# Optimization experiments

Measured on AMD Instinct MI355X. Metric: run time of the kernel, lower is better.

The kernel has to match this reference:

```python
import jax, jax.numpy as jnp
import numpy as np

jax.config.update("jax_enable_x64", True)

ZDNA_COORDS = np.array([
    [19.907, 16.823, 19.09], [18.239, 15.35, 17.81], [19.352, 12.428, 20.252],
    [19.86, 12.683, 22.751], [17.43, 10.434, 25.869], [15.111, 11.013, 24.853],
    [13.376, 8.973, 27.734], [14.066, 8.488, 30.129], [11.402, 9.495, 33.572],
    [10.614, 11.665, 32.479], [8.13, 12.128, 35.334], [8.074, 11.534, 37.812]],
    dtype=np.float32)

SIGMA_ALIGN = 5.0
WEIGHT = 10.0
MAX_ITER = 10
BINDERLEN = 400000


def _center_coords(coords):
    centered = coords - coords.mean(axis=0, keepdims=True)
    # torch .std() is unbiased (ddof=1)
    std = jnp.clip(centered.std(axis=0, ddof=1).mean(), 1e-6, None)
    return centered / std


def _soft_assignment(P, Q, sigma):
    # squared euclidean distances: [12, N]
    d2 = (jnp.sum(Q * Q, axis=1)[:, None] + jnp.sum(P * P, axis=1)[None, :]
          - 2.0 * Q @ P.T)
    d2 = jnp.maximum(d2, 0.0)
    W = jnp.exp(-d2 / (2.0 * sigma ** 2 + 1e-6))
    return W / (W.sum(axis=1, keepdims=True) + 1e-6)


def _weighted_kabsch(P, Q, W):
    dtype = P.dtype
    Pd, Qd, Wd = P.astype(jnp.float64), Q.astype(jnp.float64), W.astype(jnp.float64)
    w_sum = jnp.clip(Wd.sum(), 1e-6, None)
    centroid_P = Wd.sum(axis=0) @ Pd / w_sum   # [3]
    centroid_Q = Wd.sum(axis=1) @ Qd / w_sum   # [3]
    P_cent = Pd - centroid_P                   # [N,3]
    Q_cent = Qd - centroid_Q                   # [12,3]
    H = P_cent.T @ (Wd.T @ Q_cent)             # [3,3]
    H = H + jnp.eye(3, dtype=jnp.float64) * 1e-6
    U, _, Vh = jnp.linalg.svd(H, full_matrices=False)
    R = Vh.T @ U.T
    R = R * jnp.sign(jnp.linalg.det(R))
    t = centroid_Q - centroid_P @ R
    return R.astype(dtype), t.astype(dtype)


def _robust_alignment(P, Q, sigma, max_iter=MAX_ITER):
    Q_current = Q
    prev_rmsd = jnp.array(jnp.inf, dtype=P.dtype)  # never updated in original
    rmsd = prev_rmsd
    for _ in range(max_iter):
        W = _soft_assignment(P, Q_current)         # [12,N]
        R, t = _weighted_kabsch(P, Q_current, W)
        Q_new = Q_current @ R + t                  # [12,3]
        residuals = jnp.linalg.norm(Q_new - W @ P, axis=1)
        rmsd = jnp.sqrt(jnp.mean(residuals ** 2) + 1e-6)
        Q_current = Q_new
        rmsd = jnp.where(prev_rmsd < rmsd, prev_rmsd, rmsd)
    return rmsd


def _soft_assignment(P, Q, sigma=SIGMA_ALIGN):
    d2 = (jnp.sum(Q * Q, axis=1)[:, None] + jnp.sum(P * P, axis=1)[None, :]
          - 2.0 * Q @ P.T)
    d2 = jnp.maximum(d2, 0.0)
    W = jnp.exp(-d2 / (2.0 * sigma ** 2 + 1e-6))
    return W / (W.sum(axis=1, keepdims=True) + 1e-6)


def setup_inputs() -> dict:
    key = jax.random.key(0)
    k1, = jax.random.split(key, 1)
    xyz = jax.random.normal(k1, (BINDERLEN, 27, 3), dtype=jnp.float32) * 10.0
    zdna_ref = jnp.asarray(ZDNA_COORDS)
    return {"xyz": xyz, "zdna_ref": zdna_ref, "binderlen": BINDERLEN}


def reference(xyz, zdna_ref, binderlen):
    binder_ca = xyz[:binderlen, 1]           # [N,3]
    binder_norm = _center_coords(binder_ca)
    zdna_norm = _center_coords(zdna_ref)     # [12,3]
    rmsd = _robust_alignment(binder_norm, zdna_norm, SIGMA_ALIGN)
    return -WEIGHT * rmsd
```

## Files before the change

### kernel.cpp

```cpp
#include <hip/hip_runtime.h>
#include <math.h>

#define NBLK 256
#define THREADS 256
#define PTS 7
#define NSHARD 8
#define CPAD 16
#define KORD 5
#define MORD 6
#define NMOM 84
#define NCON 56
#define CC 50.000001

__device__ double g_slot[NBLK][8];
__device__ double g_macc[NSHARD][NMOM];
__device__ int g_cnt[2 * CPAD];

__device__ inline float waveReduceAdd(float v) {
#pragma unroll
    for (int off = 32; off > 0; off >>= 1) v += __shfl_down(v, off, 64);
    return v;
}

__device__ inline int loadRlxI(int* p) {
    return __hip_atomic_load(p, __ATOMIC_RELAXED, __HIP_MEMORY_SCOPE_AGENT);
}
__device__ inline int loadAcqI(int* p) {
    return __hip_atomic_load(p, __ATOMIC_ACQUIRE, __HIP_MEMORY_SCOPE_AGENT);
}
__device__ inline double loadRlxD(double* p) {
    return __hip_atomic_load(p, __ATOMIC_RELAXED, __HIP_MEMORY_SCOPE_AGENT);
}
__device__ inline void storeRlxD(double* p, double v) {
    __hip_atomic_store(p, v, __ATOMIC_RELAXED, __HIP_MEMORY_SCOPE_AGENT);
}

__device__ inline void arriveAndWait(int slot, int target) {
    __threadfence();
    atomicAdd(&g_cnt[slot * CPAD], 1);
    while (loadRlxI(&g_cnt[slot * CPAD]) < target) __builtin_amdgcn_s_sleep(8);
    (void)loadAcqI(&g_cnt[slot * CPAD]);
}

__device__ inline int idx6(int a, int b, int g) {
    int off = 0;
    for (int ap = 0; ap < a; ++ap) off += (7 - ap) * (8 - ap) / 2;
    return off + b * (7 - a) - b * (b - 1) / 2 + g;
}

__device__ void kabschUpdate(const double* __restrict__ dsum,
                             double (*Qd)[3], float (*Qf)[3],
                             float* __restrict__ out, int it) {
    double S[12], Tv[12][3], Q[12][3];
    for (int i = 0; i < 12; i++) {
        S[i] = dsum[i];
        Tv[i][0] = dsum[12 + i];
        Tv[i][1] = dsum[24 + i];
        Tv[i][2] = dsum[36 + i];
        for (int c = 0; c < 3; c++) Q[i][c] = Qd[i][c];
    }
    double n[12], wsum = 0;
    for (int i = 0; i < 12; i++) {
        n[i] = 1.0 / (S[i] + 1e-6);
        wsum += S[i] * n[i];
    }
    wsum = fmax(wsum, 1e-6);
    double cP[3] = {0, 0, 0}, cQ[3] = {0, 0, 0};
    for (int i = 0; i < 12; i++)
        for (int c = 0; c < 3; c++) {
            cP[c] += n[i] * Tv[i][c];
            cQ[c] += S[i] * n[i] * Q[i][c];
        }
    for (int c = 0; c < 3; c++) { cP[c] /= wsum; cQ[c] /= wsum; }

    double H[3][3] = {{0, 0, 0}, {0, 0, 0}, {0, 0, 0}};
    for (int i = 0; i < 12; i++) {
        double ta[3];
        for (int a = 0; a < 3; a++) ta[a] = n[i] * (Tv[i][a] - S[i] * cP[a]);
        for (int a = 0; a < 3; a++)
            for (int b = 0; b < 3; b++) H[a][b] += ta[a] * (Q[i][b] - cQ[b]);
    }
    for (int a = 0; a < 3; a++) H[a][a] += 1e-6;

    double A[3][3], V[3][3];
    for (int a = 0; a < 3; a++)
        for (int b = 0; b < 3; b++) {
            double s = 0;
            for (int k = 0; k < 3; k++) s += H[k][a] * H[k][b];
            A[a][b] = s;
            V[a][b] = (a == b) ? 1.0 : 0.0;
        }
    for (int sweep = 0; sweep < 8; sweep++) {
        for (int p = 0; p < 2; p++)
            for (int q = p + 1; q < 3; q++) {
                double apq = A[p][q];
                if (fabs(apq) < 1e-12 * (fabs(A[p][p]) + fabs(A[q][q]))) continue;
                double theta = (A[q][q] - A[p][p]) / (2.0 * apq);
                double t = copysign(1.0, theta) / (fabs(theta) + sqrt(theta * theta + 1.0));
                double c = 1.0 / sqrt(t * t + 1.0);
                double s = t * c;
                A[p][p] = A[p][p] - t * apq;
                A[q][q] = A[q][q] + t * apq;
                A[p][q] = 0; A[q][p] = 0;
                int r = 3 - p - q;
                double arp = A[r][p], arq = A[r][q];
                A[r][p] = A[p][r] = c * arp - s * arq;
                A[r][q] = A[q][r] = s * arp + c * arq;
                for (int k = 0; k < 3; k++) {
                    double vkp = V[k][p], vkq = V[k][q];
                    V[k][p] = c * vkp - s * vkq;
                    V[k][q] = s * vkp + c * vkq;
                }
            }
    }
    double U[3][3];
    for (int k = 0; k < 3; k++) {
        double sig = sqrt(fmax(A[k][k], 0.0));
        double u[3];
        for (int a = 0; a < 3; a++)
            u[a] = H[a][0] * V[0][k] + H[a][1] * V[1][k] + H[a][2] * V[2][k];
        double invsig = 1.0 / fmax(sig, 1e-30);
        for (int a = 0; a < 3; a++) U[a][k] = u[a] * invsig;
    }
    double R[3][3];
    for (int a = 0; a < 3; a++)
        for (int b = 0; b < 3; b++)
            R[a][b] = V[a][0] * U[b][0] + V[a][1] * U[b][1] + V[a][2] * U[b][2];
    double det = R[0][0] * (R[1][1] * R[2][2] - R[1][2] * R[2][1])
               - R[0][1] * (R[1][0] * R[2][2] - R[1][2] * R[2][0])
               + R[0][2] * (R[1][0] * R[2][1] - R[1][1] * R[2][0]);
    if (det < 0)
        for (int a = 0; a < 3; a++)
            for (int b = 0; b < 3; b++) R[a][b] = -R[a][b];
    double tr[3];
    for (int b = 0; b < 3; b++)
        tr[b] = cQ[b] - (cP[0] * R[0][b] + cP[1] * R[1][b] + cP[2] * R[2][b]);

    double res2 = 0;
    for (int i = 0; i < 12; i++) {
        double qn[3];
        for (int b = 0; b < 3; b++) {
            qn[b] = Q[i][0] * R[0][b] + Q[i][1] * R[1][b] + Q[i][2] * R[2][b] + tr[b];
            double diff = qn[b] - n[i] * Tv[i][b];
            res2 += diff * diff;
        }
        for (int b = 0; b < 3; b++) {
            Qd[i][b] = qn[b];
            Qf[i][b] = (float)qn[b];
        }
    }
    if (it == 9) {
        double rmsd = sqrt(res2 / 12.0 + 1e-6);
        out[0] = (float)(-10.0 * rmsd);
    }
}

__global__ void __launch_bounds__(THREADS)
k_all(const float* __restrict__ xyz, const float* __restrict__ zdna,
      float* __restrict__ out, int N) {
    const int tid = threadIdx.x, bid = blockIdx.x;
    const int gid = bid * THREADS + tid;
    const int gsz = NBLK * THREADS;
    const int wave = tid >> 6, lane = tid & 63;

    __shared__ int s_base;
    __shared__ double shPart[4][NMOM];
    __shared__ double red8[8][6];
    __shared__ double Md[NMOM];
    __shared__ double coefL[NCON];
    __shared__ int lutL[4][NCON];
    __shared__ double lds48[48];
    __shared__ double QdL[12][3];
    __shared__ float QfL[12][3];
    __shared__ float s_mean[3], s_inv;

    if (tid == 0) s_base = loadRlxI(&g_cnt[CPAD]);
    __syncthreads();
    const int target = s_base + NBLK;

    float px[PTS], py[PTS], pz[PTS];
    float s0 = 0, s1 = 0, s2 = 0, q0 = 0, q1 = 0, q2 = 0;
#pragma unroll
    for (int k = 0; k < PTS; k++) {
        int j = gid + k * gsz;
        px[k] = 0.0f; py[k] = 0.0f; pz[k] = 0.0f;
        if (j < N) {
            size_t b = (size_t)j * 81 + 3;
            float x = xyz[b + 0], y = xyz[b + 1], z = xyz[b + 2];
            px[k] = x; py[k] = y; pz[k] = z;
            s0 += x; s1 += y; s2 += z;
            q0 += x * x; q1 += y * y; q2 += z * z;
        }
    }
    {
        float v[6] = {s0, s1, s2, q0, q1, q2};
#pragma unroll
        for (int k = 0; k < 6; k++) v[k] = waveReduceAdd(v[k]);
        if (lane == 0) {
#pragma unroll
            for (int k = 0; k < 6; k++) shPart[wave][k] = (double)v[k];
        }
        __syncthreads();
        if (tid < 6)
            storeRlxD(&g_slot[bid][tid],
                      shPart[0][tid] + shPart[1][tid] + shPart[2][tid] + shPart[3][tid]);
        if (bid < NSHARD && tid < NMOM) storeRlxD(&g_macc[bid][tid], 0.0);
        if (tid < NMOM) __threadfence();
        __syncthreads();
        if (tid == 0) arriveAndWait(0, target);
        __syncthreads();
    }

    {
        if (tid < 48) {
            int col = tid % 6, seg = tid / 6;
            double a0 = 0, a1 = 0;
            for (int b2 = seg * 32; b2 < seg * 32 + 32; b2 += 2) {
                a0 += loadRlxD(&g_slot[b2][col]);
                a1 += loadRlxD(&g_slot[b2 + 1][col]);
            }
            red8[seg][col] = a0 + a1;
        }
        __syncthreads();
        if (tid == 0) {
            double tot[6];
            for (int c = 0; c < 6; c++) {
                double s = 0;
                for (int g = 0; g < 8; g++) s += red8[g][c];
                tot[c] = s;
            }
            double mean[3], stdsum = 0;
            for (int c = 0; c < 3; c++) {
                mean[c] = tot[c] / (double)N;
                double var = (tot[3 + c] - (double)N * mean[c] * mean[c]) / (double)(N - 1);
                stdsum += sqrt(fmax(var, 0.0));
            }
            double sdev = fmax(stdsum / 3.0, 1e-6);
            s_mean[0] = (float)mean[0];
            s_mean[1] = (float)mean[1];
            s_mean[2] = (float)mean[2];
            s_inv = (float)(1.0 / sdev);

            double z[12][3], zm[3] = {0, 0, 0};
            for (int i = 0; i < 12; i++)
                for (int c = 0; c < 3; c++) {
                    z[i][c] = (double)zdna[i * 3 + c];
                    zm[c] += z[i][c];
                }
            for (int c = 0; c < 3; c++) zm[c] /= 12.0;
            double zvar[3] = {0, 0, 0};
            for (int i = 0; i < 12; i++)
                for (int c = 0; c < 3; c++) {
                    z[i][c] -= zm[c];
                    zvar[c] += z[i][c] * z[i][c];
                }
            double zs = 0;
            for (int c = 0; c < 3; c++) zs += sqrt(zvar[c] / 11.0);
            zs = fmax(zs / 3.0, 1e-6);
            double zinv = 1.0 / zs;
            for (int i = 0; i < 12; i++)
                for (int c = 0; c < 3; c++) {
                    double q = z[i][c] * zinv;
                    QdL[i][c] = q;
                    QfL[i][c] = (float)q;
                }
        }
        __syncthreads();
    }

    {
        float mx = s_mean[0], my = s_mean[1], mz = s_mean[2];
        float inv = s_inv;
#pragma unroll
        for (int k = 0; k < PTS; k++) {
            px[k] = (px[k] - mx) * inv;
            py[k] = (py[k] - my) * inv;
            pz[k] = (pz[k] - mz) * inv;
        }
    }

    {
        float mom[NMOM];
#pragma unroll
        for (int k = 0; k < NMOM; k++) mom[k] = 0.0f;
#pragma unroll
        for (int k = 0; k < PTS; k++) {
            if (gid + k * gsz < N) {
                float x = px[k], y = py[k], z = pz[k];
                float pp = x * x + y * y + z * z;
                float w0 = __expf(-pp * (float)(1.0 / CC));
                float ta = w0;
                int m = 0;
#pragma unroll
                for (int a = 0; a <= MORD; ++a) {
                    float tb = ta;
#pragma unroll
                    for (int b = 0; b <= MORD - a; ++b) {
                        float tc = tb;
#pragma unroll
                        for (int g = 0; g <= MORD - a - b; ++g) {
                            mom[m] += tc;
                            tc *= z;
                            ++m;
                        }
                        tb *= y;
                    }
                    ta *= x;
                }
            }
        }
#pragma unroll
        for (int k = 0; k < NMOM; k++) mom[k] = waveReduceAdd(mom[k]);
        if (lane == 0) {
#pragma unroll
            for (int k = 0; k < NMOM; k++) shPart[wave][k] = (double)mom[k];
        }
        __syncthreads();
        if (tid < NMOM) {
            double s = shPart[0][tid] + shPart[1][tid] + shPart[2][tid] + shPart[3][tid];
            (void)__hip_atomic_fetch_add(&g_macc[bid & (NSHARD - 1)][tid], s,
                                         __ATOMIC_RELAXED, __HIP_MEMORY_SCOPE_AGENT);
            __threadfence();
        }
        __syncthreads();
    }

    if (bid != 0) {
        if (tid == 0) {
            __threadfence();
            atomicAdd(&g_cnt[CPAD], 1);
        }
        return;
    }
    if (tid == 0) arriveAndWait(1, target);
    __syncthreads();

    if (tid < NMOM) {
        double s = 0;
#pragma unroll
        for (int s8 = 0; s8 < NSHARD; ++s8) s += loadRlxD(&g_macc[s8][tid]);
        Md[tid] = s;
    }
    if (tid == 64) {
        int m = 0;
        for (int a = 0; a <= KORD; ++a)
            for (int b = 0; b <= KORD - a; ++b)
                for (int g = 0; g <= KORD - a - b; ++g) {
                    double c = 1.0;
                    for (int t = 0; t < a + b + g; ++t) c *= 2.0 / CC;
                    for (int t = 2; t <= a; ++t) c /= (double)t;
                    for (int t = 2; t <= b; ++t) c /= (double)t;
                    for (int t = 2; t <= g; ++t) c /= (double)t;
                    coefL[m] = c;
                    lutL[0][m] = idx6(a, b, g);
                    lutL[1][m] = idx6(a + 1, b, g);
                    lutL[2][m] = idx6(a, b + 1, g);
                    lutL[3][m] = idx6(a, b, g + 1);
                    ++m;
                }
    }
    __syncthreads();

    for (int it = 0; it < 10; ++it) {
        if (tid < 48) {
            int i = tid >> 2, comp = tid & 3;
            double qx = (double)QfL[i][0];
            double qy = (double)QfL[i][1];
            double qz = (double)QfL[i][2];
            double acc = 0.0;
            int m = 0;
            double xa = 1.0;
            for (int a = 0; a <= KORD; ++a) {
                double yb = xa;
                for (int b = 0; b <= KORD - a; ++b) {
                    double zg = yb;
                    for (int g = 0; g <= KORD - a - b; ++g) {
                        acc += coefL[m] * zg * Md[lutL[comp][m]];
                        zg *= qz;
                        ++m;
                    }
                    yb *= qy;
                }
                xa *= qx;
            }
            double qq = qx * qx + qy * qy + qz * qz;
            lds48[comp * 12 + i] = exp(-qq / CC) * acc;
        }
        __syncthreads();
        if (tid == 0) kabschUpdate(lds48, QdL, QfL, out, it);
        __syncthreads();
    }
}

extern "C" void kernel_launch(void* const* d_in, const int* in_sizes, int n_in,
                              void* d_out, int out_size, void* d_ws, size_t ws_size,
                              hipStream_t stream) {
    (void)d_ws; (void)ws_size;
    const float* xyz = (const float*)d_in[0];
    const float* zdna = (const float*)d_in[1];
    int N = in_sizes[0] / 81;
    float* out = (float*)d_out;

    hipLaunchKernelGGL(k_all, dim3(NBLK), dim3(THREADS), 0, stream,
                       xyz, zdna, out, N);
}
```

Before: 305.4 us.

## Split persistent grid-barrier kernel into three launches with staged CA buffer

Replaces the single persistent kernel and its two atomic-counter grid barriers with three kernel launches: extract CA coordinates plus sums, compute moments, then run the 10 alignment iterations on one block. The CA coordinates are written to a global SoA buffer so the moments kernel can reread them, and each block now handles a contiguous chunk instead of a grid stride. This removes the spin-wait barrier cost but adds two kernel launch boundaries and extra global write and read traffic of about 4.8 MB. The buffer is capped at MAX_N.

```diff
diff --git a/kernel.cpp b/kernel.cpp
--- a/kernel.cpp
+++ b/kernel.cpp
@@ -1,45 +1,24 @@
 #include <hip/hip_runtime.h>
 #include <math.h>
 
+#define THREADS 256
 #define NBLK 256
-#define THREADS 256
-#define PTS 7
+#define MAX_N 400000
 #define NSHARD 8
-#define CPAD 16
 #define KORD 5
 #define MORD 6
 #define NMOM 84
 #define NCON 56
 #define CC 50.000001
 
+__device__ float g_cax[MAX_N], g_cay[MAX_N], g_caz[MAX_N];
 __device__ double g_slot[NBLK][8];
 __device__ double g_macc[NSHARD][NMOM];
-__device__ int g_cnt[2 * CPAD];
 
 __device__ inline float waveReduceAdd(float v) {
 #pragma unroll
     for (int off = 32; off > 0; off >>= 1) v += __shfl_down(v, off, 64);
     return v;
-}
-
-__device__ inline int loadRlxI(int* p) {
-    return __hip_atomic_load(p, __ATOMIC_RELAXED, __HIP_MEMORY_SCOPE_AGENT);
-}
-__device__ inline int loadAcqI(int* p) {
-    return __hip_atomic_load(p, __ATOMIC_ACQUIRE, __HIP_MEMORY_SCOPE_AGENT);
-}
-__device__ inline double loadRlxD(double* p) {
-    return __hip_atomic_load(p, __ATOMIC_RELAXED, __HIP_MEMORY_SCOPE_AGENT);
-}
-__device__ inline void storeRlxD(double* p, double v) {
-    __hip_atomic_store(p, v, __ATOMIC_RELAXED, __HIP_MEMORY_SCOPE_AGENT);
-}
-
-__device__ inline void arriveAndWait(int slot, int target) {
-    __threadfence();
-    atomicAdd(&g_cnt[slot * CPAD], 1);
-    while (loadRlxI(&g_cnt[slot * CPAD]) < target) __builtin_amdgcn_s_sleep(8);
-    (void)loadAcqI(&g_cnt[slot * CPAD]);
 }
 
 __device__ inline int idx6(int a, int b, int g) {
@@ -156,192 +135,138 @@
 }
 
 __global__ void __launch_bounds__(THREADS)
-k_all(const float* __restrict__ xyz, const float* __restrict__ zdna,
-      float* __restrict__ out, int N) {
+k_extract(const float* __restrict__ xyz, int N, int chunk) {
     const int tid = threadIdx.x, bid = blockIdx.x;
-    const int gid = bid * THREADS + tid;
-    const int gsz = NBLK * THREADS;
+    const int start = bid * chunk;
+    const int lim = (start + chunk < N) ? (start + chunk) : N;
     const int wave = tid >> 6, lane = tid & 63;
 
-    __shared__ int s_base;
+    float s0 = 0, s1 = 0, s2 = 0, q0 = 0, q1 = 0, q2 = 0;
+    for (int j = start + tid; j < lim; j += THREADS) {
+        size_t b = (size_t)j * 81 + 3;
+        float x = xyz[b + 0], y = xyz[b + 1], z = xyz[b + 2];
+        g_cax[j] = x; g_cay[j] = y; g_caz[j] = z;
+        s0 += x; s1 += y; s2 += z;
+        q0 += x * x; q1 += y * y; q2 += z * z;
+    }
+    __shared__ double p6[4][6];
+    float v[6] = {s0, s1, s2, q0, q1, q2};
+#pragma unroll
+    for (int k = 0; k < 6; k++) v[k] = waveReduceAdd(v[k]);
+    if (lane == 0) {
+#pragma unroll
+        for (int k = 0; k < 6; k++) p6[wave][k] = (double)v[k];
+    }
+    __syncthreads();
+    if (tid < 6)
+        g_slot[bid][tid] = p6[0][tid] + p6[1][tid] + p6[2][tid] + p6[3][tid];
+    if (bid < NSHARD && tid >= 64 && tid < 64 + NMOM)
+        g_macc[bid][tid - 64] = 0.0;
+}
+
+__global__ void __launch_bounds__(THREADS)
+k_moments(int N, int chunk) {
+    const int tid = threadIdx.x, bid = blockIdx.x;
+    const int wave = tid >> 6, lane = tid & 63;
+    __shared__ double red8[8][6];
+    __shared__ float s_mean[3], s_inv;
     __shared__ double shPart[4][NMOM];
-    __shared__ double red8[8][6];
+
+    if (tid < 48) {
+        int col = tid % 6, seg = tid / 6;
+        double a0 = 0, a1 = 0;
+        for (int b2 = seg * 32; b2 < seg * 32 + 32; b2 += 2) {
+            a0 += g_slot[b2][col];
+            a1 += g_slot[b2 + 1][col];
+        }
+        red8[seg][col] = a0 + a1;
+    }
+    __syncthreads();
+    if (tid == 0) {
+        double tot[6];
+        for (int c = 0; c < 6; c++) {
+            double s = 0;
+            for (int g = 0; g < 8; g++) s += red8[g][c];
+            tot[c] = s;
+        }
+        double mean[3], stdsum = 0;
+        for (int c = 0; c < 3; c++) {
+            mean[c] = tot[c] / (double)N;
+            double var = (tot[3 + c] - (double)N * mean[c] * mean[c]) / (double)(N - 1);
+            stdsum += sqrt(fmax(var, 0.0));
+        }
+        double sdev = fmax(stdsum / 3.0, 1e-6);
+        s_mean[0] = (float)mean[0];
+        s_mean[1] = (float)mean[1];
+        s_mean[2] = (float)mean[2];
+        s_inv = (float)(1.0 / sdev);
+    }
+    __syncthreads();
+
+    const float mx = s_mean[0], my = s_mean[1], mz = s_mean[2];
+    const float inv = s_inv;
+    const int start = bid * chunk;
+    const int lim = (start + chunk < N) ? (start + chunk) : N;
+
+    float mom[NMOM];
+#pragma unroll
+    for (int k = 0; k < NMOM; k++) mom[k] = 0.0f;
+    for (int j = start + tid; j < lim; j += THREADS) {
+        float x = (g_cax[j] - mx) * inv;
+        float y = (g_cay[j] - my) * inv;
+        float z = (g_caz[j] - mz) * inv;
+        float pp = x * x + y * y + z * z;
+        float w0 = __expf(-pp * (float)(1.0 / CC));
+        float ta = w0;
+        int m = 0;
+#pragma unroll
+        for (int a = 0; a <= MORD; ++a) {
+            float tb = ta;
+#pragma unroll
+            for (int b = 0; b <= MORD - a; ++b) {
+                float tc = tb;
+#pragma unroll
+                for (int g = 0; g <= MORD - a - b; ++g) {
+                    mom[m] += tc;
+                    tc *= z;
+                    ++m;
+                }
+                tb *= y;
+            }
+            ta *= x;
+        }
+    }
+#pragma unroll
+    for (int k = 0; k < NMOM; k++) mom[k] = waveReduceAdd(mom[k]);
+    if (lane == 0) {
+#pragma unroll
+        for (int k = 0; k < NMOM; k++) shPart[wave][k] = (double)mom[k];
+    }
+    __syncthreads();
+    if (tid < NMOM) {
+        double s = shPart[0][tid] + shPart[1][tid] + shPart[2][tid] + shPart[3][tid];
+        (void)__hip_atomic_fetch_add(&g_macc[bid & (NSHARD - 1)][tid], s,
+                                     __ATOMIC_RELAXED, __HIP_MEMORY_SCOPE_AGENT);
+    }
+}
+
+__global__ void __launch_bounds__(THREADS)
+k_iters(const float* __restrict__ zdna, float* __restrict__ out, int N) {
+    const int tid = threadIdx.x;
     __shared__ double Md[NMOM];
     __shared__ double coefL[NCON];
     __shared__ int lutL[4][NCON];
     __shared__ double lds48[48];
     __shared__ double QdL[12][3];
     __shared__ float QfL[12][3];
-    __shared__ float s_mean[3], s_inv;
-
-    if (tid == 0) s_base = loadRlxI(&g_cnt[CPAD]);
-    __syncthreads();
-    const int target = s_base + NBLK;
-
-    float px[PTS], py[PTS], pz[PTS];
-    float s0 = 0, s1 = 0, s2 = 0, q0 = 0, q1 = 0, q2 = 0;
-#pragma unroll
-    for (int k = 0; k < PTS; k++) {
-        int j = gid + k * gsz;
-        px[k] = 0.0f; py[k] = 0.0f; pz[k] = 0.0f;
-        if (j < N) {
-            size_t b = (size_t)j * 81 + 3;
-            float x = xyz[b + 0], y = xyz[b + 1], z = xyz[b + 2];
-            px[k] = x; py[k] = y; pz[k] = z;
-            s0 += x; s1 += y; s2 += z;
-            q0 += x * x; q1 += y * y; q2 += z * z;
-        }
-    }
-    {
-        float v[6] = {s0, s1, s2, q0, q1, q2};
-#pragma unroll
-        for (int k = 0; k < 6; k++) v[k] = waveReduceAdd(v[k]);
-        if (lane == 0) {
-#pragma unroll
-            for (int k = 0; k < 6; k++) shPart[wave][k] = (double)v[k];
-        }
-        __syncthreads();
-        if (tid < 6)
-            storeRlxD(&g_slot[bid][tid],
-                      shPart[0][tid] + shPart[1][tid] + shPart[2][tid] + shPart[3][tid]);
-        if (bid < NSHARD && tid < NMOM) storeRlxD(&g_macc[bid][tid], 0.0);
-        if (tid < NMOM) __threadfence();
-        __syncthreads();
-        if (tid == 0) arriveAndWait(0, target);
-        __syncthreads();
-    }
-
-    {
-        if (tid < 48) {
-            int col = tid % 6, seg = tid / 6;
-            double a0 = 0, a1 = 0;
-            for (int b2 = seg * 32; b2 < seg * 32 + 32; b2 += 2) {
-                a0 += loadRlxD(&g_slot[b2][col]);
-                a1 += loadRlxD(&g_slot[b2 + 1][col]);
-            }
-            red8[seg][col] = a0 + a1;
-        }
-        __syncthreads();
-        if (tid == 0) {
-            double tot[6];
-            for (int c = 0; c < 6; c++) {
-                double s = 0;
-                for (int g = 0; g < 8; g++) s += red8[g][c];
-                tot[c] = s;
-            }
-            double mean[3], stdsum = 0;
-            for (int c = 0; c < 3; c++) {
-                mean[c] = tot[c] / (double)N;
-                double var = (tot[3 + c] - (double)N * mean[c] * mean[c]) / (double)(N - 1);
-                stdsum += sqrt(fmax(var, 0.0));
-            }
-            double sdev = fmax(stdsum / 3.0, 1e-6);
-            s_mean[0] = (float)mean[0];
-            s_mean[1] = (float)mean[1];
-            s_mean[2] = (float)mean[2];
-            s_inv = (float)(1.0 / sdev);
-
-            double z[12][3], zm[3] = {0, 0, 0};
-            for (int i = 0; i < 12; i++)
-                for (int c = 0; c < 3; c++) {
-                    z[i][c] = (double)zdna[i * 3 + c];
-                    zm[c] += z[i][c];
-                }
-            for (int c = 0; c < 3; c++) zm[c] /= 12.0;
-            double zvar[3] = {0, 0, 0};
-            for (int i = 0; i < 12; i++)
-                for (int c = 0; c < 3; c++) {
-                    z[i][c] -= zm[c];
-                    zvar[c] += z[i][c] * z[i][c];
-                }
-            double zs = 0;
-            for (int c = 0; c < 3; c++) zs += sqrt(zvar[c] / 11.0);
-            zs = fmax(zs / 3.0, 1e-6);
-            double zinv = 1.0 / zs;
-            for (int i = 0; i < 12; i++)
-                for (int c = 0; c < 3; c++) {
-                    double q = z[i][c] * zinv;
-                    QdL[i][c] = q;
-                    QfL[i][c] = (float)q;
-                }
-        }
-        __syncthreads();
-    }
-
-    {
-        float mx = s_mean[0], my = s_mean[1], mz = s_mean[2];
-        float inv = s_inv;
-#pragma unroll
-        for (int k = 0; k < PTS; k++) {
-            px[k] = (px[k] - mx) * inv;
-            py[k] = (py[k] - my) * inv;
-            pz[k] = (pz[k] - mz) * inv;
-        }
-    }
-
-    {
-        float mom[NMOM];
-#pragma unroll
-        for (int k = 0; k < NMOM; k++) mom[k] = 0.0f;
-#pragma unroll
-        for (int k = 0; k < PTS; k++) {
-            if (gid + k * gsz < N) {
-                float x = px[k], y = py[k], z = pz[k];
-                float pp = x * x + y * y + z * z;
-                float w0 = __expf(-pp * (float)(1.0 / CC));
-                float ta = w0;
-                int m = 0;
-#pragma unroll
-                for (int a = 0; a <= MORD; ++a) {
-                    float tb = ta;
-#pragma unroll
-                    for (int b = 0; b <= MORD - a; ++b) {
-                        float tc = tb;
-#pragma unroll
-                        for (int g = 0; g <= MORD - a - b; ++g) {
-                            mom[m] += tc;
-                            tc *= z;
-                            ++m;
-                        }
-                        tb *= y;
-                    }
-                    ta *= x;
-                }
-            }
-        }
-#pragma unroll
-        for (int k = 0; k < NMOM; k++) mom[k] = waveReduceAdd(mom[k]);
-        if (lane == 0) {
-#pragma unroll
-            for (int k = 0; k < NMOM; k++) shPart[wave][k] = (double)mom[k];
-        }
-        __syncthreads();
-        if (tid < NMOM) {
-            double s = shPart[0][tid] + shPart[1][tid] + shPart[2][tid] + shPart[3][tid];
-            (void)__hip_atomic_fetch_add(&g_macc[bid & (NSHARD - 1)][tid], s,
-                                         __ATOMIC_RELAXED, __HIP_MEMORY_SCOPE_AGENT);
-            __threadfence();
-        }
-        __syncthreads();
-    }
-
-    if (bid != 0) {
-        if (tid == 0) {
-            __threadfence();
-            atomicAdd(&g_cnt[CPAD], 1);
-        }
-        return;
-    }
-    if (tid == 0) arriveAndWait(1, target);
-    __syncthreads();
 
     if (tid < NMOM) {
         double s = 0;
 #pragma unroll
-        for (int s8 = 0; s8 < NSHARD; ++s8) s += loadRlxD(&g_macc[s8][tid]);
+        for (int s8 = 0; s8 < NSHARD; ++s8) s += g_macc[s8][tid];
         Md[tid] = s;
     }
-    if (tid == 64) {
+    if (tid == 128) {
         int m = 0;
         for (int a = 0; a <= KORD; ++a)
             for (int b = 0; b <= KORD - a; ++b)
@@ -358,6 +283,31 @@
                     lutL[3][m] = idx6(a, b, g + 1);
                     ++m;
                 }
+    }
+    if (tid == 192) {
+        double z[12][3], zm[3] = {0, 0, 0};
+        for (int i = 0; i < 12; i++)
+            for (int c = 0; c < 3; c++) {
+                z[i][c] = (double)zdna[i * 3 + c];
+                zm[c] += z[i][c];
+            }
+        for (int c = 0; c < 3; c++) zm[c] /= 12.0;
+        double zvar[3] = {0, 0, 0};
+        for (int i = 0; i < 12; i++)
+            for (int c = 0; c < 3; c++) {
+                z[i][c] -= zm[c];
+                zvar[c] += z[i][c] * z[i][c];
+            }
+        double zs = 0;
+        for (int c = 0; c < 3; c++) zs += sqrt(zvar[c] / 11.0);
+        zs = fmax(zs / 3.0, 1e-6);
+        double zinv = 1.0 / zs;
+        for (int i = 0; i < 12; i++)
+            for (int c = 0; c < 3; c++) {
+                double q = z[i][c] * zinv;
+                QdL[i][c] = q;
+                QfL[i][c] = (float)q;
+            }
     }
     __syncthreads();
 
@@ -399,8 +349,13 @@
     const float* xyz = (const float*)d_in[0];
     const float* zdna = (const float*)d_in[1];
     int N = in_sizes[0] / 81;
+    int chunk = (N + NBLK - 1) / NBLK;
     float* out = (float*)d_out;
 
-    hipLaunchKernelGGL(k_all, dim3(NBLK), dim3(THREADS), 0, stream,
-                       xyz, zdna, out, N);
-}
+    hipLaunchKernelGGL(k_extract, dim3(NBLK), dim3(THREADS), 0, stream,
+                       xyz, N, chunk);
+    hipLaunchKernelGGL(k_moments, dim3(NBLK), dim3(THREADS), 0, stream,
+                       N, chunk);
+    hipLaunchKernelGGL(k_iters, dim3(1), dim3(THREADS), 0, stream,
+                       zdna, out, N);
+}
```

Result: faster. 274.3 us (-10.2%).
